# Kernel tuning notes

Hardware: AMD Instinct MI355X
Metric: run time of the kernel (lower is better)

Reference implementation:

```python
import jax, jax.numpy as jnp
import numpy as np

N, DIM, EDGE_DIM, HEADS, EXP_HEADS, E = 50000, 64, 32, 8, 16, 800000
HEAD_DIM = DIM // HEADS
SCALE = HEAD_DIM ** -0.5
EPS = 1e-16


def setup_inputs() -> dict:
    key = jax.random.key(0)
    ks = jax.random.split(key, 16)
    s = DIM ** -0.5
    return {
        "x": jax.random.normal(ks[0], (N, DIM), jnp.float32),
        "edges": jax.random.normal(ks[1], (E, EDGE_DIM), jnp.float32),
        "edge_index": jax.random.randint(ks[2], (2, E), 0, N, jnp.int64),
        "Wq": jax.random.normal(ks[3], (DIM, DIM), jnp.float32) * s,
        "Wk": jax.random.normal(ks[4], (DIM, DIM), jnp.float32) * s,
        "Wv": jax.random.normal(ks[5], (DIM, DIM), jnp.float32) * s,
        "Wek": jax.random.normal(ks[6], (EDGE_DIM, DIM), jnp.float32) * (EDGE_DIM ** -0.5),
        "Wev": jax.random.normal(ks[7], (EDGE_DIM, DIM), jnp.float32) * (EDGE_DIM ** -0.5),
        "Wexp": jax.random.normal(ks[8], (HEADS, EXP_HEADS), jnp.float32) * (HEADS ** -0.5),
        "Wsq": jax.random.normal(ks[9], (EXP_HEADS, HEADS), jnp.float32) * (EXP_HEADS ** -0.5),
        "bsq": jax.random.normal(ks[10], (HEADS,), jnp.float32) * 0.01,
        "Wout": jax.random.normal(ks[11], (DIM, DIM), jnp.float32) * s,
        "bout": jax.random.normal(ks[12], (DIM,), jnp.float32) * 0.01,
        "temperature": jnp.full((1,), 0.01, jnp.float32),
    }


def reference(x, edges, edge_index, Wq, Wk, Wv, Wek, Wev, Wexp, Wsq, bsq, Wout, bout, temperature):
    n = x.shape[0]
    dst = edge_index[0]  # segment / query index
    src = edge_index[1]  # key/value gather index

    q = (x @ Wq).reshape(n, HEADS, HEAD_DIM)      # [n,h,d]
    k = (x @ Wk).reshape(n, HEADS, HEAD_DIM)
    v = (x @ Wv).reshape(n, HEADS, HEAD_DIM)      # v_non_scatter

    qe = q[dst]                                   # [E,h,d] edge gathers
    ke = k[src]
    ve = v[src]

    edge_k = (edges @ Wek).reshape(-1, HEADS, HEAD_DIM)
    edge_v = (edges @ Wev).reshape(-1, HEADS, HEAD_DIM)

    ke = (ke + edge_k) * SCALE
    attn = jnp.einsum('ehd,ehd->eh', qe, ke) / temperature[0]  # [E,h]
    attn = attn @ Wexp                                          # [E,eh]

    # sparse (segment) softmax over edges grouped by dst, per expanded head
    mx = jax.ops.segment_max(attn, dst, num_segments=n)         # [n,eh]
    ex = jnp.exp(attn - mx[dst])
    sm = jax.ops.segment_sum(ex, dst, num_segments=n)
    attn = ex / (sm[dst] + EPS)

    attn = attn @ Wsq + bsq                                     # [E,h]

    ve = ve + edge_v
    out_e = attn[:, :, None] * ve                               # [E,h,d]
    agg = jax.ops.segment_sum(out_e, dst, num_segments=n)       # [n,h,d]

    out = (v - agg).reshape(n, DIM)                             # graph Laplacian: v - aggregated
    out = out @ Wout + bout
    return out, attn.T  # attention returned as [h, E]
```

## Files before the change

kernel.cpp:

```cpp
#include <hip/hip_runtime.h>

#define N_NODES 50000
#define DIM 64
#define EDGE_DIM 32
#define HEADS 8
#define EXP_HEADS 16
#define NEDGE 800000
#define SCALE 0.35355339059327373f
#define EPS 1e-16f
#define NEG_BIG -1e30f
#define NB_SCAN ((N_NODES + 255) / 256)

#define RFL(x) __builtin_amdgcn_readfirstlane(x)

__global__ __launch_bounds__(256) void qkv_kernel(
    const float* __restrict__ x, const float* __restrict__ Wq,
    const float* __restrict__ Wk, const float* __restrict__ Wv,
    float* __restrict__ q, float* __restrict__ k, float* __restrict__ v) {
    int gid = blockIdx.x * 256 + threadIdx.x;
    if (gid >= (N_NODES / 4) * DIM) return;
    int quad = gid >> 6, j = gid & 63;
    long i0 = (long)quad * 4;
    float aq[4] = {0,0,0,0}, ak[4] = {0,0,0,0}, av[4] = {0,0,0,0};
#pragma unroll
    for (int l = 0; l < DIM; ++l) {
        float wq = Wq[l * DIM + j], wk = Wk[l * DIM + j], wv = Wv[l * DIM + j];
#pragma unroll
        for (int r = 0; r < 4; ++r) {
            float xv = x[(i0 + r) * DIM + l];
            aq[r] = fmaf(xv, wq, aq[r]);
            ak[r] = fmaf(xv, wk, ak[r]);
            av[r] = fmaf(xv, wv, av[r]);
        }
    }
#pragma unroll
    for (int r = 0; r < 4; ++r) {
        q[(i0 + r) * DIM + j] = aq[r];
        k[(i0 + r) * DIM + j] = ak[r];
        v[(i0 + r) * DIM + j] = av[r];
    }
}

__global__ __launch_bounds__(256) void hist_kernel(
    const int* __restrict__ eidx, unsigned* __restrict__ cnt) {
    int e = blockIdx.x * 256 + threadIdx.x;
    if (e >= NEDGE) return;
    atomicAdd(&cnt[eidx[e]], 1u);
}

__global__ __launch_bounds__(256) void scan_reduce(
    const unsigned* __restrict__ cnt, unsigned* __restrict__ blocksum) {
    int gid = blockIdx.x * 256 + threadIdx.x;
    unsigned v = (gid < N_NODES) ? cnt[gid] : 0u;
    v += __shfl_xor(v, 1);  v += __shfl_xor(v, 2);
    v += __shfl_xor(v, 4);  v += __shfl_xor(v, 8);
    v += __shfl_xor(v, 16); v += __shfl_xor(v, 32);
    __shared__ unsigned ws4[4];
    if ((threadIdx.x & 63) == 0) ws4[threadIdx.x >> 6] = v;
    __syncthreads();
    if (threadIdx.x == 0)
        blocksum[blockIdx.x] = ws4[0] + ws4[1] + ws4[2] + ws4[3];
}

__global__ __launch_bounds__(256) void scan_base(
    const unsigned* __restrict__ blocksum, unsigned* __restrict__ blockbase) {
    __shared__ unsigned ps[256];
    int t = threadIdx.x;
    unsigned v = (t < NB_SCAN) ? blocksum[t] : 0u;
    ps[t] = v;
    __syncthreads();
    for (int off = 1; off < 256; off <<= 1) {
        unsigned val = (t >= off) ? ps[t - off] : 0u;
        __syncthreads();
        ps[t] += val;
        __syncthreads();
    }
    blockbase[t] = ps[t] - v;
}

__global__ __launch_bounds__(256) void scan_final(
    const unsigned* __restrict__ cnt, const unsigned* __restrict__ blockbase,
    unsigned* __restrict__ offsets, unsigned* __restrict__ cursor) {
    __shared__ unsigned ps[256];
    int t = threadIdx.x;
    int gid = blockIdx.x * 256 + t;
    unsigned v = (gid < N_NODES) ? cnt[gid] : 0u;
    ps[t] = v;
    __syncthreads();
    for (int off = 1; off < 256; off <<= 1) {
        unsigned val = (t >= off) ? ps[t - off] : 0u;
        __syncthreads();
        ps[t] += val;
        __syncthreads();
    }
    unsigned off_ = blockbase[blockIdx.x] + ps[t] - v;
    if (gid < N_NODES) { offsets[gid] = off_; cursor[gid] = off_; }
    if (gid == N_NODES - 1) offsets[N_NODES] = off_ + v;
}

__global__ __launch_bounds__(256) void scatter_kernel(
    const int* __restrict__ eidx, unsigned* __restrict__ cursor,
    unsigned* __restrict__ perm, unsigned* __restrict__ iperm,
    unsigned* __restrict__ srcs, unsigned* __restrict__ dsts) {
    int e = blockIdx.x * 256 + threadIdx.x;
    if (e >= NEDGE) return;
    int dst = eidx[e];
    unsigned pos = atomicAdd(&cursor[dst], 1u);
    perm[pos] = e;
    iperm[e] = pos;
    srcs[pos] = (unsigned)eidx[NEDGE + e];
    dsts[pos] = (unsigned)dst;
}

#define WARM_BLOCKS 2048
__global__ __launch_bounds__(256) void warm_kernel(
    const float4* __restrict__ src, float* __restrict__ dummy) {
    const long n4 = (long)NEDGE * EDGE_DIM / 4;
    long i = (long)blockIdx.x * 256 + threadIdx.x;
    const long stride = (long)WARM_BLOCKS * 256;
    float acc = 0.f;
    for (; i < n4; i += stride) {
        float4 t = src[i];
        acc += t.x + t.y + t.z + t.w;
    }
    dummy[(long)blockIdx.x * 256 + threadIdx.x] = acc;
}

__global__ __launch_bounds__(256) void edge_attn_kernel(
    const float* __restrict__ edges,
    const float* __restrict__ q, const float* __restrict__ k,
    const float* __restrict__ Wek,
    const float* __restrict__ temp, const unsigned* __restrict__ perm,
    const unsigned* __restrict__ offsets, const unsigned* __restrict__ srcs,
    float* __restrict__ logit8) {
    int tid = threadIdx.x;
    int w = tid >> 6, lane = tid & 63;
    int h = lane >> 3, d = lane & 7;
    float wekr[4][8];
#pragma unroll
    for (int j = 0; j < 4; ++j)
#pragma unroll
        for (int i = 0; i < 8; ++i)
            wekr[j][i] = Wek[(d * 4 + j) * DIM + h * 8 + i];
    float invt = SCALE / temp[0];
    int n = blockIdx.x * 4 + w;
    unsigned nb = offsets[n];
    int deg = (int)(offsets[n + 1] - nb);
    const float* __restrict__ qp = q + (long)n * DIM;
    float qreg = qp[lane];
    float qv[8];
#pragma unroll
    for (int t = 0; t < 8; ++t) qv[t] = qp[h * 8 + t];
    float g0 = 0.f, g1 = 0.f, g2 = 0.f, g3 = 0.f;
#pragma unroll
    for (int t = 0; t < 8; ++t) {
        g0 = fmaf(qv[t], wekr[0][t], g0);
        g1 = fmaf(qv[t], wekr[1][t], g1);
        g2 = fmaf(qv[t], wekr[2][t], g2);
        g3 = fmaf(qv[t], wekr[3][t], g3);
    }
    int j = 0;
    for (; j + 4 <= deg; j += 4) {
        float p[4];
#pragma unroll
        for (int g2i = 0; g2i < 4; ++g2i) {
            long slot = (long)nb + j + g2i;
            int e_g = RFL((int)perm[slot]);
            int s_g = RFL((int)srcs[slot]);
            float kv = k[(long)s_g * DIM + lane];
            float4 ed = *(const float4*)(edges + (long)e_g * EDGE_DIM + d * 4);
            float pp = qreg * kv;
            pp = fmaf(g0, ed.x, pp);
            pp = fmaf(g1, ed.y, pp);
            pp = fmaf(g2, ed.z, pp);
            pp = fmaf(g3, ed.w, pp);
            p[g2i] = pp;
        }
#pragma unroll
        for (int i = 0; i < 4; ++i) p[i] += __shfl_xor(p[i], 1);
#pragma unroll
        for (int i = 0; i < 4; ++i) p[i] += __shfl_xor(p[i], 2);
#pragma unroll
        for (int i = 0; i < 4; ++i) p[i] += __shfl_xor(p[i], 4);
        if (d == 0) {
#pragma unroll
            for (int i = 0; i < 4; ++i)
                logit8[((long)nb + j + i) * HEADS + h] = p[i] * invt;
        }
    }
    for (; j < deg; ++j) {
        long slot = (long)nb + j;
        int e_g = RFL((int)perm[slot]);
        int s_g = RFL((int)srcs[slot]);
        float kv = k[(long)s_g * DIM + lane];
        float4 ed = *(const float4*)(edges + (long)e_g * EDGE_DIM + d * 4);
        float pp = qreg * kv;
        pp = fmaf(g0, ed.x, pp);
        pp = fmaf(g1, ed.y, pp);
        pp = fmaf(g2, ed.z, pp);
        pp = fmaf(g3, ed.w, pp);
        pp += __shfl_xor(pp, 1);
        pp += __shfl_xor(pp, 2);
        pp += __shfl_xor(pp, 4);
        if (d == 0) logit8[slot * HEADS + h] = pp * invt;
    }
}

__global__ __launch_bounds__(256) void stats_kernel(
    const float* __restrict__ logit8, const unsigned* __restrict__ offsets,
    const float* __restrict__ Wexp, float2* __restrict__ stats) {
    int gid = blockIdx.x * 256 + threadIdx.x;
    if (gid >= N_NODES * EXP_HEADS) return;
    int n = gid >> 4, eh = gid & 15;
    float we[HEADS];
#pragma unroll
    for (int hh = 0; hh < HEADS; ++hh) we[hh] = Wexp[hh * EXP_HEADS + eh];
    unsigned nb = offsets[n];
    int deg = (int)(offsets[n + 1] - nb);
    float m = NEG_BIG, s = 0.f;
    for (int j = 0; j < deg; ++j) {
        const float4* lp = (const float4*)(logit8 + (long)(nb + j) * HEADS);
        float4 l0 = lp[0], l1 = lp[1];
        float a = l0.x * we[0];
        a = fmaf(l0.y, we[1], a); a = fmaf(l0.z, we[2], a); a = fmaf(l0.w, we[3], a);
        a = fmaf(l1.x, we[4], a); a = fmaf(l1.y, we[5], a);
        a = fmaf(l1.z, we[6], a); a = fmaf(l1.w, we[7], a);
        float mn = fmaxf(m, a);
        s = s * __expf(m - mn) + __expf(a - mn);
        m = mn;
    }
    float2 st; st.x = m; st.y = 1.f / (s + EPS);
    stats[gid] = st;
}

__global__ __launch_bounds__(256) void a8_kernel(
    const float* __restrict__ logit8, const unsigned* __restrict__ dsts,
    const float2* __restrict__ stats, const float* __restrict__ Wexp,
    const float* __restrict__ Wsq,
    const float* __restrict__ bsq, float* __restrict__ a8s) {
    int tid = threadIdx.x;
    int w = tid >> 6, lane = tid & 63;
    int g = lane >> 4, t16 = lane & 15;
    long slot0 = ((long)blockIdx.x * 4 + w) * 4;
    float we[HEADS];
#pragma unroll
    for (int hh = 0; hh < HEADS; ++hh) we[hh] = Wexp[hh * EXP_HEADS + t16];
    float wsq[HEADS];
#pragma unroll
    for (int j = 0; j < HEADS; ++j) wsq[j] = Wsq[t16 * HEADS + j];
    int hmap = 4 * (t16 & 1) + 2 * ((t16 >> 1) & 1) + ((t16 >> 2) & 1);
    float bs_w = bsq[hmap];
    bool b0 = (t16 & 1), b1 = (t16 & 2), b2 = (t16 & 4);

    const float4* lp = (const float4*)(logit8 + (slot0 + g) * HEADS);
    float4 l0 = lp[0], l1 = lp[1];
    float a = l0.x * we[0];
    a = fmaf(l0.y, we[1], a); a = fmaf(l0.z, we[2], a); a = fmaf(l0.w, we[3], a);
    a = fmaf(l1.x, we[4], a); a = fmaf(l1.y, we[5], a);
    a = fmaf(l1.z, we[6], a); a = fmaf(l1.w, we[7], a);
    int dstg = (int)dsts[slot0 + g];
    float2 st = stats[(long)dstg * EXP_HEADS + t16];
    float p = __expf(a - st.x) * st.y;
    float v0 = p * wsq[0], v1 = p * wsq[1], v2 = p * wsq[2], v3 = p * wsq[3];
    float v4 = p * wsq[4], v5 = p * wsq[5], v6 = p * wsq[6], v7 = p * wsq[7];
    float q0, q1, q2, q3, n0, n1, s8;
    q0 = (b0 ? v4 : v0) + __shfl_xor(b0 ? v0 : v4, 1);
    q1 = (b0 ? v5 : v1) + __shfl_xor(b0 ? v1 : v5, 1);
    q2 = (b0 ? v6 : v2) + __shfl_xor(b0 ? v2 : v6, 1);
    q3 = (b0 ? v7 : v3) + __shfl_xor(b0 ? v3 : v7, 1);
    n0 = (b1 ? q2 : q0) + __shfl_xor(b1 ? q0 : q2, 2);
    n1 = (b1 ? q3 : q1) + __shfl_xor(b1 ? q1 : q3, 2);
    s8 = (b2 ? n1 : n0) + __shfl_xor(b2 ? n0 : n1, 4);
    float a8sum = s8 + __shfl_xor(s8, 8);
    if (t16 < 8) a8s[(slot0 + g) * HEADS + hmap] = a8sum + bs_w;
}

__global__ __launch_bounds__(256) void agg_kernel(
    const float* __restrict__ edges, const float* __restrict__ v,
    const float* __restrict__ a8s,
    const unsigned* __restrict__ offsets, const unsigned* __restrict__ perm,
    const unsigned* __restrict__ srcs,
    const float* __restrict__ Wev, float* __restrict__ vmagg) {
    int tid = threadIdx.x;
    int w = tid >> 6, lane = tid & 63;
    int h = lane >> 3, d = lane & 7;
    int n = blockIdx.x * 4 + w;
    unsigned nb = offsets[n];
    int deg = (int)(offsets[n + 1] - nb);
    float acc = 0.f, t0 = 0.f, t1 = 0.f, t2 = 0.f, t3 = 0.f;
    int j = 0;
    for (; j + 4 <= deg; j += 4) {
#pragma unroll
        for (int g2 = 0; g2 < 4; ++g2) {
            long slot = (long)nb + j + g2;
            int e_g = RFL((int)perm[slot]);
            int s_g = RFL((int)srcs[slot]);
            float a8 = a8s[slot * HEADS + h];
            float vv = v[(long)s_g * DIM + lane];
            float4 ed = *(const float4*)(edges + (long)e_g * EDGE_DIM + d * 4);
            acc = fmaf(a8, vv, acc);
            t0 = fmaf(a8, ed.x, t0);
            t1 = fmaf(a8, ed.y, t1);
            t2 = fmaf(a8, ed.z, t2);
            t3 = fmaf(a8, ed.w, t3);
        }
    }
    for (; j < deg; ++j) {
        long slot = (long)nb + j;
        int e_g = RFL((int)perm[slot]);
        int s_g = RFL((int)srcs[slot]);
        float a8 = a8s[slot * HEADS + h];
        float vv = v[(long)s_g * DIM + lane];
        float4 ed = *(const float4*)(edges + (long)e_g * EDGE_DIM + d * 4);
        acc = fmaf(a8, vv, acc);
        t0 = fmaf(a8, ed.x, t0);
        t1 = fmaf(a8, ed.y, t1);
        t2 = fmaf(a8, ed.z, t2);
        t3 = fmaf(a8, ed.w, t3);
    }
    float ev = 0.f;
#pragma unroll
    for (int l = 0; l < EDGE_DIM; ++l) {
        float tv = ((l & 3) == 0) ? t0 : ((l & 3) == 1) ? t1 : ((l & 3) == 2) ? t2 : t3;
        float tl = __shfl(tv, h * 8 + (l >> 2));
        ev = fmaf(tl, Wev[l * DIM + lane], ev);
    }
    vmagg[(long)n * DIM + lane] = v[(long)n * DIM + lane] - (acc + ev);
}

__global__ __launch_bounds__(256) void transpose_kernel(
    const float* __restrict__ a8s, const unsigned* __restrict__ iperm,
    float* __restrict__ out2) {
    int e = blockIdx.x * 256 + threadIdx.x;
    if (e >= NEDGE) return;
    long sj = iperm[e];
    const float4* p = (const float4*)(a8s + sj * HEADS);
    float4 lo = p[0], hi = p[1];
    out2[0L * NEDGE + e] = lo.x; out2[1L * NEDGE + e] = lo.y;
    out2[2L * NEDGE + e] = lo.z; out2[3L * NEDGE + e] = lo.w;
    out2[4L * NEDGE + e] = hi.x; out2[5L * NEDGE + e] = hi.y;
    out2[6L * NEDGE + e] = hi.z; out2[7L * NEDGE + e] = hi.w;
}

__global__ __launch_bounds__(256) void out_kernel(
    const float* __restrict__ vmagg, const float* __restrict__ Wout,
    const float* __restrict__ bout, float* __restrict__ out) {
    int gid = blockIdx.x * 256 + threadIdx.x;
    if (gid >= (N_NODES / 4) * DIM) return;
    int quad = gid >> 6, j = gid & 63;
    long i0 = (long)quad * 4;
    float b = bout[j];
    float ac[4] = {b, b, b, b};
#pragma unroll
    for (int l = 0; l < DIM; ++l) {
        float wv = Wout[l * DIM + j];
#pragma unroll
        for (int r = 0; r < 4; ++r)
            ac[r] = fmaf(vmagg[(i0 + r) * DIM + l], wv, ac[r]);
    }
#pragma unroll
    for (int r = 0; r < 4; ++r) out[(i0 + r) * DIM + j] = ac[r];
}

extern "C" void kernel_launch(void* const* d_in, const int* in_sizes, int n_in,
                              void* d_out, int out_size, void* d_ws, size_t ws_size,
                              hipStream_t stream) {
    const float* x     = (const float*)d_in[0];
    const float* edges = (const float*)d_in[1];
    const int*   eidx  = (const int*)d_in[2];
    const float* Wq    = (const float*)d_in[3];
    const float* Wk    = (const float*)d_in[4];
    const float* Wv    = (const float*)d_in[5];
    const float* Wek   = (const float*)d_in[6];
    const float* Wev   = (const float*)d_in[7];
    const float* Wexp  = (const float*)d_in[8];
    const float* Wsq   = (const float*)d_in[9];
    const float* bsq   = (const float*)d_in[10];
    const float* Wout  = (const float*)d_in[11];
    const float* bout  = (const float*)d_in[12];
    const float* temp  = (const float*)d_in[13];

    float* ws = (float*)d_ws;
    float* q       = ws;
    float* k       = q + (long)N_NODES * DIM;
    float* v       = k + (long)N_NODES * DIM;
    float* logit8  = v + (long)N_NODES * DIM;
    float* vmagg   = logit8 + (long)NEDGE * EXP_HEADS;
    float* a8s     = q;
    float2*   stats  = (float2*)vmagg;
    unsigned* dsts   = (unsigned*)(vmagg + 1600000L);
    unsigned* perm    = (unsigned*)(vmagg + (long)N_NODES * DIM);
    unsigned* iperm   = perm + NEDGE;
    unsigned* srcs    = iperm + NEDGE;
    unsigned* cnt     = srcs + NEDGE;
    unsigned* offsets = cnt + N_NODES;
    unsigned* cursor  = offsets + N_NODES + 1;
    unsigned* blocksum  = cursor + N_NODES;
    unsigned* blockbase = blocksum + 256;

    hipMemsetAsync(cnt, 0, (size_t)N_NODES * sizeof(unsigned), stream);

    float* out1 = (float*)d_out;
    float* out2 = out1 + (long)N_NODES * DIM;

    qkv_kernel<<<(N_NODES / 4 * DIM + 255) / 256, 256, 0, stream>>>(x, Wq, Wk, Wv, q, k, v);
    hist_kernel<<<(NEDGE + 255) / 256, 256, 0, stream>>>(eidx, cnt);
    scan_reduce<<<NB_SCAN, 256, 0, stream>>>(cnt, blocksum);
    scan_base<<<1, 256, 0, stream>>>(blocksum, blockbase);
    scan_final<<<NB_SCAN, 256, 0, stream>>>(cnt, blockbase, offsets, cursor);
    warm_kernel<<<WARM_BLOCKS, 256, 0, stream>>>((const float4*)edges, logit8);
    scatter_kernel<<<(NEDGE + 255) / 256, 256, 0, stream>>>(eidx, cursor, perm, iperm, srcs, dsts);
    edge_attn_kernel<<<N_NODES / 4, 256, 0, stream>>>(edges, q, k, Wek, temp,
                                                      perm, offsets, srcs, logit8);
    stats_kernel<<<(N_NODES * EXP_HEADS + 255) / 256, 256, 0, stream>>>(logit8, offsets, Wexp, stats);
    a8_kernel<<<NEDGE / 16, 256, 0, stream>>>(logit8, dsts, stats, Wexp, Wsq, bsq, a8s);
    agg_kernel<<<N_NODES / 4, 256, 0, stream>>>(edges, v, a8s, offsets, perm, srcs, Wev, vmagg);
    transpose_kernel<<<(NEDGE + 255) / 256, 256, 0, stream>>>(a8s, iperm, out2);
    out_kernel<<<(N_NODES / 4 * DIM + 255) / 256, 256, 0, stream>>>(vmagg, Wout, bout, out1);
}
```

Before: 450.7 us.

## Fuse softmax stats, attention projection and aggregation into one per-node kernel

Replaces the stats, a8 and agg kernels with a single per-node wavefront kernel. Each wave computes the online softmax max/sum for its node's edges, then recomputes the probabilities, projects them through Wsq, writes a8s and accumulates the weighted values in the same pass. This removes two launches, the stats and dsts buffers and the a8s re-read, at the cost of reading logit8 twice per node. It also leaves lanes idle on low-degree nodes, since work is now per node instead of per edge.

```diff
diff --git a/kernel.cpp b/kernel.cpp
--- a/kernel.cpp
+++ b/kernel.cpp
@@ -101,7 +101,7 @@
 __global__ __launch_bounds__(256) void scatter_kernel(
     const int* __restrict__ eidx, unsigned* __restrict__ cursor,
     unsigned* __restrict__ perm, unsigned* __restrict__ iperm,
-    unsigned* __restrict__ srcs, unsigned* __restrict__ dsts) {
+    unsigned* __restrict__ srcs) {
     int e = blockIdx.x * 256 + threadIdx.x;
     if (e >= NEDGE) return;
     int dst = eidx[e];
@@ -109,7 +109,6 @@
     perm[pos] = e;
     iperm[e] = pos;
     srcs[pos] = (unsigned)eidx[NEDGE + e];
-    dsts[pos] = (unsigned)dst;
 }
 
 #define WARM_BLOCKS 2048
@@ -206,117 +205,95 @@
     }
 }
 
-__global__ __launch_bounds__(256) void stats_kernel(
-    const float* __restrict__ logit8, const unsigned* __restrict__ offsets,
-    const float* __restrict__ Wexp, float2* __restrict__ stats) {
-    int gid = blockIdx.x * 256 + threadIdx.x;
-    if (gid >= N_NODES * EXP_HEADS) return;
-    int n = gid >> 4, eh = gid & 15;
+__global__ __launch_bounds__(256) void node_fused_kernel(
+    const float* __restrict__ edges, const float* __restrict__ v,
+    const float* __restrict__ logit8,
+    const unsigned* __restrict__ offsets, const unsigned* __restrict__ perm,
+    const unsigned* __restrict__ srcs,
+    const float* __restrict__ Wexp, const float* __restrict__ Wsq,
+    const float* __restrict__ bsq, const float* __restrict__ Wev,
+    float* __restrict__ a8s, float* __restrict__ vmagg) {
+    int tid = threadIdx.x;
+    int w = tid >> 6, lane = tid & 63;
+    int g = lane >> 4, t16 = lane & 15;
+    int h = lane >> 3, d = lane & 7;
     float we[HEADS];
 #pragma unroll
-    for (int hh = 0; hh < HEADS; ++hh) we[hh] = Wexp[hh * EXP_HEADS + eh];
+    for (int hh = 0; hh < HEADS; ++hh) we[hh] = Wexp[hh * EXP_HEADS + t16];
+    float wsq[HEADS];
+#pragma unroll
+    for (int j = 0; j < HEADS; ++j) wsq[j] = Wsq[t16 * HEADS + j];
+    int hmap = 4 * (t16 & 1) + 2 * ((t16 >> 1) & 1) + ((t16 >> 2) & 1);
+    int ih = ((h >> 2) & 1) | (((h >> 1) & 1) << 1) | ((h & 1) << 2);
+    float bs_h = bsq[h], bs_w = bsq[hmap];
+    bool b0 = (t16 & 1), b1 = (t16 & 2), b2 = (t16 & 4);
+
+    int n = blockIdx.x * 4 + w;
     unsigned nb = offsets[n];
     int deg = (int)(offsets[n + 1] - nb);
+
     float m = NEG_BIG, s = 0.f;
-    for (int j = 0; j < deg; ++j) {
-        const float4* lp = (const float4*)(logit8 + (long)(nb + j) * HEADS);
+    for (int j0 = 0; j0 < deg; j0 += 4) {
+        const float4* lp = (const float4*)(logit8 + ((long)nb + j0 + g) * HEADS);
         float4 l0 = lp[0], l1 = lp[1];
         float a = l0.x * we[0];
         a = fmaf(l0.y, we[1], a); a = fmaf(l0.z, we[2], a); a = fmaf(l0.w, we[3], a);
         a = fmaf(l1.x, we[4], a); a = fmaf(l1.y, we[5], a);
         a = fmaf(l1.z, we[6], a); a = fmaf(l1.w, we[7], a);
-        float mn = fmaxf(m, a);
-        s = s * __expf(m - mn) + __expf(a - mn);
+        if (j0 + g < deg) {
+            float mn = fmaxf(m, a);
+            s = s * __expf(m - mn) + __expf(a - mn);
+            m = mn;
+        }
+    }
+#pragma unroll
+    for (int off = 16; off < 64; off <<= 1) {
+        float m2 = __shfl_xor(m, off), s2 = __shfl_xor(s, off);
+        float mn = fmaxf(m, m2);
+        s = s * __expf(m - mn) + s2 * __expf(m2 - mn);
         m = mn;
     }
-    float2 st; st.x = m; st.y = 1.f / (s + EPS);
-    stats[gid] = st;
-}
-
-__global__ __launch_bounds__(256) void a8_kernel(
-    const float* __restrict__ logit8, const unsigned* __restrict__ dsts,
-    const float2* __restrict__ stats, const float* __restrict__ Wexp,
-    const float* __restrict__ Wsq,
-    const float* __restrict__ bsq, float* __restrict__ a8s) {
-    int tid = threadIdx.x;
-    int w = tid >> 6, lane = tid & 63;
-    int g = lane >> 4, t16 = lane & 15;
-    long slot0 = ((long)blockIdx.x * 4 + w) * 4;
-    float we[HEADS];
-#pragma unroll
-    for (int hh = 0; hh < HEADS; ++hh) we[hh] = Wexp[hh * EXP_HEADS + t16];
-    float wsq[HEADS];
-#pragma unroll
-    for (int j = 0; j < HEADS; ++j) wsq[j] = Wsq[t16 * HEADS + j];
-    int hmap = 4 * (t16 & 1) + 2 * ((t16 >> 1) & 1) + ((t16 >> 2) & 1);
-    float bs_w = bsq[hmap];
-    bool b0 = (t16 & 1), b1 = (t16 & 2), b2 = (t16 & 4);
-
-    const float4* lp = (const float4*)(logit8 + (slot0 + g) * HEADS);
-    float4 l0 = lp[0], l1 = lp[1];
-    float a = l0.x * we[0];
-    a = fmaf(l0.y, we[1], a); a = fmaf(l0.z, we[2], a); a = fmaf(l0.w, we[3], a);
-    a = fmaf(l1.x, we[4], a); a = fmaf(l1.y, we[5], a);
-    a = fmaf(l1.z, we[6], a); a = fmaf(l1.w, we[7], a);
-    int dstg = (int)dsts[slot0 + g];
-    float2 st = stats[(long)dstg * EXP_HEADS + t16];
-    float p = __expf(a - st.x) * st.y;
-    float v0 = p * wsq[0], v1 = p * wsq[1], v2 = p * wsq[2], v3 = p * wsq[3];
-    float v4 = p * wsq[4], v5 = p * wsq[5], v6 = p * wsq[6], v7 = p * wsq[7];
-    float q0, q1, q2, q3, n0, n1, s8;
-    q0 = (b0 ? v4 : v0) + __shfl_xor(b0 ? v0 : v4, 1);
-    q1 = (b0 ? v5 : v1) + __shfl_xor(b0 ? v1 : v5, 1);
-    q2 = (b0 ? v6 : v2) + __shfl_xor(b0 ? v2 : v6, 1);
-    q3 = (b0 ? v7 : v3) + __shfl_xor(b0 ? v3 : v7, 1);
-    n0 = (b1 ? q2 : q0) + __shfl_xor(b1 ? q0 : q2, 2);
-    n1 = (b1 ? q3 : q1) + __shfl_xor(b1 ? q1 : q3, 2);
-    s8 = (b2 ? n1 : n0) + __shfl_xor(b2 ? n0 : n1, 4);
-    float a8sum = s8 + __shfl_xor(s8, 8);
-    if (t16 < 8) a8s[(slot0 + g) * HEADS + hmap] = a8sum + bs_w;
-}
-
-__global__ __launch_bounds__(256) void agg_kernel(
-    const float* __restrict__ edges, const float* __restrict__ v,
-    const float* __restrict__ a8s,
-    const unsigned* __restrict__ offsets, const unsigned* __restrict__ perm,
-    const unsigned* __restrict__ srcs,
-    const float* __restrict__ Wev, float* __restrict__ vmagg) {
-    int tid = threadIdx.x;
-    int w = tid >> 6, lane = tid & 63;
-    int h = lane >> 3, d = lane & 7;
-    int n = blockIdx.x * 4 + w;
-    unsigned nb = offsets[n];
-    int deg = (int)(offsets[n + 1] - nb);
+    float rs = 1.f / (s + EPS);
+
     float acc = 0.f, t0 = 0.f, t1 = 0.f, t2 = 0.f, t3 = 0.f;
-    int j = 0;
-    for (; j + 4 <= deg; j += 4) {
-#pragma unroll
-        for (int g2 = 0; g2 < 4; ++g2) {
-            long slot = (long)nb + j + g2;
-            int e_g = RFL((int)perm[slot]);
-            int s_g = RFL((int)srcs[slot]);
-            float a8 = a8s[slot * HEADS + h];
-            float vv = v[(long)s_g * DIM + lane];
-            float4 ed = *(const float4*)(edges + (long)e_g * EDGE_DIM + d * 4);
-            acc = fmaf(a8, vv, acc);
-            t0 = fmaf(a8, ed.x, t0);
-            t1 = fmaf(a8, ed.y, t1);
-            t2 = fmaf(a8, ed.z, t2);
-            t3 = fmaf(a8, ed.w, t3);
-        }
-    }
-    for (; j < deg; ++j) {
-        long slot = (long)nb + j;
-        int e_g = RFL((int)perm[slot]);
-        int s_g = RFL((int)srcs[slot]);
-        float a8 = a8s[slot * HEADS + h];
-        float vv = v[(long)s_g * DIM + lane];
-        float4 ed = *(const float4*)(edges + (long)e_g * EDGE_DIM + d * 4);
-        acc = fmaf(a8, vv, acc);
-        t0 = fmaf(a8, ed.x, t0);
-        t1 = fmaf(a8, ed.y, t1);
-        t2 = fmaf(a8, ed.z, t2);
-        t3 = fmaf(a8, ed.w, t3);
+    for (int j0 = 0; j0 < deg; j0 += 4) {
+        int cnt = deg - j0; if (cnt > 4) cnt = 4;
+        const float4* lp = (const float4*)(logit8 + ((long)nb + j0 + g) * HEADS);
+        float4 l0 = lp[0], l1 = lp[1];
+        float a = l0.x * we[0];
+        a = fmaf(l0.y, we[1], a); a = fmaf(l0.z, we[2], a); a = fmaf(l0.w, we[3], a);
+        a = fmaf(l1.x, we[4], a); a = fmaf(l1.y, we[5], a);
+        a = fmaf(l1.z, we[6], a); a = fmaf(l1.w, we[7], a);
+        float p = (g < cnt) ? __expf(a - m) * rs : 0.f;
+        float v0 = p * wsq[0], v1 = p * wsq[1], v2 = p * wsq[2], v3 = p * wsq[3];
+        float v4 = p * wsq[4], v5 = p * wsq[5], v6 = p * wsq[6], v7 = p * wsq[7];
+        float q0, q1, q2, q3, n0, n1, s8;
+        q0 = (b0 ? v4 : v0) + __shfl_xor(b0 ? v0 : v4, 1);
+        q1 = (b0 ? v5 : v1) + __shfl_xor(b0 ? v1 : v5, 1);
+        q2 = (b0 ? v6 : v2) + __shfl_xor(b0 ? v2 : v6, 1);
+        q3 = (b0 ? v7 : v3) + __shfl_xor(b0 ? v3 : v7, 1);
+        n0 = (b1 ? q2 : q0) + __shfl_xor(b1 ? q0 : q2, 2);
+        n1 = (b1 ? q3 : q1) + __shfl_xor(b1 ? q1 : q3, 2);
+        s8 = (b2 ? n1 : n0) + __shfl_xor(b2 ? n0 : n1, 4);
+        float a8sum = s8 + __shfl_xor(s8, 8);
+        if (t16 < 8 && g < cnt)
+            a8s[((long)nb + j0 + g) * HEADS + hmap] = a8sum + bs_w;
+#pragma unroll
+        for (int i = 0; i < 4; ++i) {
+            if (i < cnt) {
+                long slot = (long)nb + j0 + i;
+                int e_g = RFL((int)perm[slot]);
+                int s_g = RFL((int)srcs[slot]);
+                float a8 = __shfl(a8sum, i * 16 + ih) + bs_h;
+                float vv = v[(long)s_g * DIM + lane];
+                float4 ed = *(const float4*)(edges + (long)e_g * EDGE_DIM + d * 4);
+                acc = fmaf(a8, vv, acc);
+                t0 = fmaf(a8, ed.x, t0);
+                t1 = fmaf(a8, ed.y, t1);
+                t2 = fmaf(a8, ed.z, t2);
+                t3 = fmaf(a8, ed.w, t3);
+            }
+        }
     }
     float ev = 0.f;
 #pragma unroll
@@ -387,8 +364,6 @@
     float* logit8  = v + (long)N_NODES * DIM;
     float* vmagg   = logit8 + (long)NEDGE * EXP_HEADS;
     float* a8s     = q;
-    float2*   stats  = (float2*)vmagg;
-    unsigned* dsts   = (unsigned*)(vmagg + 1600000L);
     unsigned* perm    = (unsigned*)(vmagg + (long)N_NODES * DIM);
     unsigned* iperm   = perm + NEDGE;
     unsigned* srcs    = iperm + NEDGE;
@@ -409,12 +384,11 @@
     scan_base<<<1, 256, 0, stream>>>(blocksum, blockbase);
     scan_final<<<NB_SCAN, 256, 0, stream>>>(cnt, blockbase, offsets, cursor);
     warm_kernel<<<WARM_BLOCKS, 256, 0, stream>>>((const float4*)edges, logit8);
-    scatter_kernel<<<(NEDGE + 255) / 256, 256, 0, stream>>>(eidx, cursor, perm, iperm, srcs, dsts);
+    scatter_kernel<<<(NEDGE + 255) / 256, 256, 0, stream>>>(eidx, cursor, perm, iperm, srcs);
     edge_attn_kernel<<<N_NODES / 4, 256, 0, stream>>>(edges, q, k, Wek, temp,
                                                       perm, offsets, srcs, logit8);
-    stats_kernel<<<(N_NODES * EXP_HEADS + 255) / 256, 256, 0, stream>>>(logit8, offsets, Wexp, stats);
-    a8_kernel<<<NEDGE / 16, 256, 0, stream>>>(logit8, dsts, stats, Wexp, Wsq, bsq, a8s);
-    agg_kernel<<<N_NODES / 4, 256, 0, stream>>>(edges, v, a8s, offsets, perm, srcs, Wev, vmagg);
+    node_fused_kernel<<<N_NODES / 4, 256, 0, stream>>>(edges, v, logit8, offsets, perm, srcs,
+                                                       Wexp, Wsq, bsq, Wev, a8s, vmagg);
     transpose_kernel<<<(NEDGE + 255) / 256, 256, 0, stream>>>(a8s, iperm, out2);
     out_kernel<<<(N_NODES / 4 * DIM + 255) / 256, 256, 0, stream>>>(vmagg, Wout, bout, out1);
 }
```

Result: no change. 451.7 us (+0.2%).
